# Optimization experiments

Hardware: AMD Instinct MI355X
Metric: run time of the kernel (lower is better)

Reference implementation:

```python
import jax, jax.numpy as jnp
import numpy as np

N = 100000       # num nodes
E = 1600000      # num edges (before self loops)
IN = 128         # in_channels
H = 4            # heads (layer 1)
C = 64           # hidden_channels
BN_EPS = 1e-5
NEG_SLOPE = 0.2  # PyG GATConv default


def setup_inputs() -> dict:
    key = jax.random.key(0)
    ks = jax.random.split(key, 12)
    s = lambda k, shape: jax.random.normal(k, shape, jnp.float32) * 0.05
    return {
        "x": jax.random.normal(ks[0], (N, IN), jnp.float32),
        "edge_index": jax.random.randint(ks[1], (2, E), 0, N),
        # GATConv layer 1: in=128 -> 64 per head, 4 heads, concat
        "W1": s(ks[2], (IN, H * C)),
        "a_src1": s(ks[3], (H, C)),
        "a_dst1": s(ks[4], (H, C)),
        "b1": jnp.zeros((H * C,), jnp.float32),
        # BatchNorm1d(256), eval mode with default running stats
        "bn_gamma": jnp.ones((H * C,), jnp.float32),
        "bn_beta": jnp.zeros((H * C,), jnp.float32),
        # GATConv layer 2: 256 -> 1, heads=1, concat=False
        "W2": s(ks[5], (H * C, 1)),
        "a_src2": s(ks[6], (1, 1)),
        "a_dst2": s(ks[7], (1, 1)),
        "b2": jnp.zeros((1,), jnp.float32),
        # risk predictor MLP: Linear(1,64) -> ReLU -> Linear(64,1) -> Sigmoid
        "mlp_w1": s(ks[8], (1, C)),
        "mlp_b1": jnp.zeros((C,), jnp.float32),
        "mlp_w2": s(ks[9], (C, 1)),
        "mlp_b2": jnp.zeros((1,), jnp.float32),
    }


def gat_conv(x, W, a_s, a_d, b, src, dst, n, concat):
    """PyG-style GATConv (self loops already appended to src/dst)."""
    h_, c_ = a_s.shape
    h = (x @ W).reshape(n, h_, c_)                       # [N,H,C]
    alpha_src = jnp.einsum('nhc,hc->nh', h, a_s)          # [N,H]
    alpha_dst = jnp.einsum('nhc,hc->nh', h, a_d)          # [N,H]
    alpha = jax.nn.leaky_relu(alpha_src[src] + alpha_dst[dst], NEG_SLOPE)  # [E,H]
    # segment softmax over destination nodes (self loops guarantee nonempty segments)
    amax = jax.ops.segment_max(alpha, dst, num_segments=n)
    ex = jnp.exp(alpha - amax[dst])
    den = jax.ops.segment_sum(ex, dst, num_segments=n)
    coef = ex / den[dst]                                  # [E,H]
    out = jax.ops.segment_sum(h[src] * coef[..., None], dst, num_segments=n)  # [N,H,C]
    out = out.reshape(n, h_ * c_) if concat else out.mean(axis=1)
    return out + b


def reference(x, edge_index, W1, a_src1, a_dst1, b1, bn_gamma, bn_beta,
              W2, a_src2, a_dst2, b2, mlp_w1, mlp_b1, mlp_w2, mlp_b2):
    n = x.shape[0]
    loops = jnp.arange(n)
    src = jnp.concatenate([edge_index[0], loops])
    dst = jnp.concatenate([edge_index[1], loops])

    h = gat_conv(x, W1, a_src1, a_dst1, b1, src, dst, n, concat=True)   # [N,256]
    # BatchNorm1d eval: running_mean=0, running_var=1
    h = h / jnp.sqrt(jnp.float32(1.0 + BN_EPS)) * bn_gamma + bn_beta
    h = jax.nn.elu(h)
    # dropout is identity in eval mode
    h = gat_conv(h, W2, a_src2, a_dst2, b2, src, dst, n, concat=False)  # [N,1]

    risk = jax.nn.relu(h @ mlp_w1 + mlp_b1)
    risk = jax.nn.sigmoid(risk @ mlp_w2 + mlp_b2)                        # [N,1]
    return risk
```

## Files before the change

### kernel.cpp

```cpp
#include <hip/hip_runtime.h>
#include <math.h>

#define NSL 0.2f
#define BSH 8
#define CAP 4608
#define ECHUNK 4096
#define MAXNB 512

typedef __attribute__((ext_vector_type(8))) short bf16x8;
typedef __attribute__((ext_vector_type(4))) float f32x4;
typedef __attribute__((ext_vector_type(2))) float floatx2;

__device__ __forceinline__ unsigned short f2b(float f){
  unsigned int u = __builtin_bit_cast(unsigned int, f);
  u = (u + 0x7FFFu + ((u >> 16) & 1u)) >> 16;
  return (unsigned short)u;
}
__device__ __forceinline__ unsigned cvtpk_bf16(float a, float b){
  unsigned r; asm("v_cvt_pk_bf16_f32 %0, %1, %2" : "=v"(r) : "v"(a), "v"(b)); return r;
}
__device__ __forceinline__ void pkfma(floatx2& a, floatx2 x, floatx2 w){
  asm("v_pk_fma_f32 %0, %1, %2, %0" : "+v"(a) : "v"(x), "v"(w));
}

__global__ void k_binit(int* gCur, int NB){
  int i = blockIdx.x*blockDim.x + threadIdx.x;
  if (i < NB) gCur[i] = i*CAP;
}

__global__ __launch_bounds__(256) void k_bucket(const int* __restrict__ esrc, const int* __restrict__ edst,
                                                int E, int NB, int* gCur, uint2* __restrict__ ebuf){
  __shared__ int hist[MAXNB];
  __shared__ int base[MAXNB];
  int t = threadIdx.x;
  for (int i=t;i<NB;i+=256) hist[i] = 0;
  __syncthreads();
  int e0 = blockIdx.x*ECHUNK;
  int srcv[16], dstv[16];
  #pragma unroll
  for (int j=0;j<16;j++){
    int e = e0 + t + j*256;
    if (e < E){ srcv[j] = esrc[e]; dstv[j] = edst[e]; atomicAdd(&hist[dstv[j]>>BSH], 1); }
    else dstv[j] = -1;
  }
  __syncthreads();
  for (int i=t;i<NB;i+=256){
    int h = hist[i];
    base[i] = h > 0 ? atomicAdd(&gCur[i], h) : 0;
    hist[i] = 0;
  }
  __syncthreads();
  #pragma unroll
  for (int j=0;j<16;j++){
    if (dstv[j] >= 0){
      int b = dstv[j]>>BSH;
      int pos = base[b] + atomicAdd(&hist[b], 1);
      if (pos < (b+1)*CAP)
        ebuf[pos] = (uint2){ (unsigned)srcv[j], (unsigned)dstv[j] };
    }
  }
}

__global__ __launch_bounds__(256) void k_csr(const int* __restrict__ gCur, const uint2* __restrict__ ebuf,
                                             int* __restrict__ rows, int* __restrict__ deg,
                                             int* __restrict__ csr, int N){
  __shared__ int lcnt[256];
  __shared__ int rofs[256];
  __shared__ int csr_l[CAP+256];
  int b = blockIdx.x, t = threadIdx.x;
  int node0 = b<<BSH;
  int nNodes = min(256, N - node0);
  int cnt_b = min(gCur[b] - b*CAP, CAP);
  lcnt[t] = 0;
  __syncthreads();
  const uint2* eb = ebuf + (size_t)b*CAP;
  for (int i=t;i<cnt_b;i+=256) atomicAdd(&lcnt[eb[i].y & 255], 1);
  __syncthreads();
  int v = (t < nNodes) ? (lcnt[t] + 1) : 0;
  rofs[t] = v; __syncthreads();
  #pragma unroll
  for (int o=1;o<256;o<<=1){
    int x = (t>=o) ? rofs[t-o] : 0; __syncthreads();
    rofs[t] += x; __syncthreads();
  }
  int excl = rofs[t] - v;
  if (t < nNodes) csr_l[excl] = node0 + t;
  lcnt[t] = excl + 1;
  __syncthreads();
  for (int i=t;i<cnt_b;i+=256){
    uint2 e = eb[i];
    int pos = atomicAdd(&lcnt[e.y & 255], 1);
    csr_l[pos] = (int)e.x;
  }
  __syncthreads();
  int total = rofs[255];
  int gbase = b*(CAP+256);
  for (int i=t;i<total;i+=256) csr[gbase+i] = csr_l[i];
  if (t < nNodes){ rows[node0+t] = gbase + excl; deg[node0+t] = v; }
}

__global__ __launch_bounds__(256) void k_prep_w(const float* __restrict__ W, unsigned short* __restrict__ wt){
  int idx = blockIdx.x*256 + threadIdx.x;
  int k = idx >> 8, ch = idx & 255;
  wt[ch*128 + k] = f2b(W[idx]);
}

__global__ __launch_bounds__(256) void k_gemm1(const unsigned short* __restrict__ w1t,
                                               const float* __restrict__ x,
                                               const float* __restrict__ a_s1,
                                               const float* __restrict__ a_d1,
                                               unsigned char* __restrict__ h1f8,
                                               float* __restrict__ asrc, float* __restrict__ adst,
                                               int N){
  __shared__ unsigned short xs[64][132];
  int tid = threadIdx.x;
  int lane = tid & 63, w = tid >> 6;
  int g = lane >> 4, nr = lane & 15;
  int n0 = blockIdx.x*64;

  #pragma unroll
  for (int i=0;i<8;i++){
    int idx = tid + i*256;
    int node = idx >> 5, c4 = idx & 31;
    int gn = n0 + node;
    float4 v = (gn < N) ? *(const float4*)&x[(size_t)gn*128 + c4*4] : make_float4(0,0,0,0);
    uint2 pk = { cvtpk_bf16(v.x, v.y), cvtpk_bf16(v.z, v.w) };
    *(uint2*)&xs[node][c4*4] = pk;
  }
  __syncthreads();

  int node_f[4]; bool val_f[4];
  #pragma unroll
  for (int fn=0;fn<4;fn++){ node_f[fn] = n0 + fn*16 + nr; val_f[fn] = node_f[fn] < N; }

  f32x4 acc[4][4] = {};
  #pragma unroll
  for (int s=0;s<4;s++){
    int ks = s*32;
    bf16x8 af[4], bf[4];
    #pragma unroll
    for (int fm=0;fm<4;fm++){
      int ch = w*64 + fm*16 + nr;
      const ushort4 lo = *(const ushort4*)(w1t + ch*128 + ks + 4*g);
      const ushort4 hi = *(const ushort4*)(w1t + ch*128 + ks + 16 + 4*g);
      af[fm] = (bf16x8){ (short)lo.x,(short)lo.y,(short)lo.z,(short)lo.w,
                         (short)hi.x,(short)hi.y,(short)hi.z,(short)hi.w };
    }
    #pragma unroll
    for (int fn=0;fn<4;fn++){
      union { uint2 u2[2]; bf16x8 v; } bb;
      bb.u2[0] = *(const uint2*)&xs[fn*16 + nr][ks + 4*g];
      bb.u2[1] = *(const uint2*)&xs[fn*16 + nr][ks + 16 + 4*g];
      bf[fn] = bb.v;
    }
    #pragma unroll
    for (int fm=0;fm<4;fm++)
      #pragma unroll
      for (int fn=0;fn<4;fn++)
        acc[fm][fn] = __builtin_amdgcn_mfma_f32_16x16x32_bf16(af[fm], bf[fn], acc[fm][fn], 0, 0, 0);
  }

  float ps[4] = {0.f,0.f,0.f,0.f}, pd[4] = {0.f,0.f,0.f,0.f};
  #pragma unroll
  for (int fm=0;fm<4;fm++){
    int cb = w*64 + fm*16 + g*4;
    float4 av = *(const float4*)&a_s1[cb];
    float4 dv = *(const float4*)&a_d1[cb];
    #pragma unroll
    for (int fn=0;fn<4;fn++){
      f32x4 c = acc[fm][fn];
      if (val_f[fn]){
        int u = __builtin_amdgcn_cvt_pk_fp8_f32(c[0], c[1], 0, false);
        u = __builtin_amdgcn_cvt_pk_fp8_f32(c[2], c[3], u, true);
        *(unsigned int*)(h1f8 + (size_t)node_f[fn]*256 + cb) = (unsigned int)u;
      }
      ps[fn] += c[0]*av.x + c[1]*av.y + c[2]*av.z + c[3]*av.w;
      pd[fn] += c[0]*dv.x + c[1]*dv.y + c[2]*dv.z + c[3]*dv.w;
    }
  }
  #pragma unroll
  for (int fn=0;fn<4;fn++){
    ps[fn] += __shfl_xor(ps[fn], 16); ps[fn] += __shfl_xor(ps[fn], 32);
    pd[fn] += __shfl_xor(pd[fn], 16); pd[fn] += __shfl_xor(pd[fn], 32);
    if (g == 0 && val_f[fn]){
      asrc[node_f[fn]*4 + w] = ps[fn];
      adst[node_f[fn]*4 + w] = pd[fn];
    }
  }
}

__global__ __launch_bounds__(256) void k_agg1(const int* __restrict__ rows, const int* __restrict__ deg,
                                              const int* __restrict__ csr,
                                              const unsigned char* __restrict__ h1f8,
                                              const float* __restrict__ asrc, const float* __restrict__ adst,
                                              const float* __restrict__ b1,
                                              const float* __restrict__ gamma, const float* __restrict__ beta,
                                              const float* __restrict__ W2,
                                              float* __restrict__ h2, int N){
  int lane = threadIdx.x & 63, wv = threadIdx.x >> 6;
  int node = blockIdx.x*4 + wv;
  if (node >= N) return;
  int slot = lane >> 4, l4 = lane & 15;
  int head = l4 >> 2;
  int rs = rows[node], d = deg[node];
  float adh = adst[node*4 + head];
  const uint4* h1u4 = (const uint4*)h1f8;
  floatx2 acc2[8];
  #pragma unroll
  for (int j=0;j<8;j++){ acc2[j][0] = 0.f; acc2[j][1] = 0.f; }
  float den = 0.f;
  int i = slot;
  if (i < d){
    int s = csr[rs+i];
    float aa = asrc[s*4 + head];
    uint4 v = h1u4[(size_t)s*16 + l4];
    while (true){
      int in = i + 4;
      bool hn = in < d;
      int sn = hn ? csr[rs+in] : 0;
      float al = aa + adh;
      al = fmaxf(al, NSL*al);
      float wgt = __expf(al);
      den += wgt;
      floatx2 ww; ww[0] = wgt; ww[1] = wgt;
      floatx2 f;
      f = __builtin_amdgcn_cvt_pk_f32_fp8(v.x, false); pkfma(acc2[0], f, ww);
      f = __builtin_amdgcn_cvt_pk_f32_fp8(v.x, true ); pkfma(acc2[1], f, ww);
      f = __builtin_amdgcn_cvt_pk_f32_fp8(v.y, false); pkfma(acc2[2], f, ww);
      f = __builtin_amdgcn_cvt_pk_f32_fp8(v.y, true ); pkfma(acc2[3], f, ww);
      f = __builtin_amdgcn_cvt_pk_f32_fp8(v.z, false); pkfma(acc2[4], f, ww);
      f = __builtin_amdgcn_cvt_pk_f32_fp8(v.z, true ); pkfma(acc2[5], f, ww);
      f = __builtin_amdgcn_cvt_pk_f32_fp8(v.w, false); pkfma(acc2[6], f, ww);
      f = __builtin_amdgcn_cvt_pk_f32_fp8(v.w, true ); pkfma(acc2[7], f, ww);
      if (!hn) break;
      i = in;
      aa = asrc[sn*4 + head];
      v = h1u4[(size_t)sn*16 + l4];
    }
  }
  #pragma unroll
  for (int j=0;j<8;j++){
    acc2[j][0] += __shfl_xor(acc2[j][0],16); acc2[j][1] += __shfl_xor(acc2[j][1],16);
    acc2[j][0] += __shfl_xor(acc2[j][0],32); acc2[j][1] += __shfl_xor(acc2[j][1],32);
  }
  den += __shfl_xor(den,16); den += __shfl_xor(den,32);
  float inv = 1.f/den;
  const float bsc = 0.99999500003749968f;
  int c = l4*16;
  float p = 0.f;
  #pragma unroll
  for (int q=0;q<4;q++){
    int cq = c + q*4;
    float4 bb = *(const float4*)&b1[cq];
    float4 gg = *(const float4*)&gamma[cq];
    float4 be = *(const float4*)&beta[cq];
    float4 w2 = *(const float4*)&W2[cq];
    float o0 = (acc2[q*2+0][0]*inv + bb.x)*bsc*gg.x + be.x;
    float o1 = (acc2[q*2+0][1]*inv + bb.y)*bsc*gg.y + be.y;
    float o2 = (acc2[q*2+1][0]*inv + bb.z)*bsc*gg.z + be.z;
    float o3 = (acc2[q*2+1][1]*inv + bb.w)*bsc*gg.w + be.w;
    o0 = (o0>0.f)?o0:(__expf(o0)-1.f); o1 = (o1>0.f)?o1:(__expf(o1)-1.f);
    o2 = (o2>0.f)?o2:(__expf(o2)-1.f); o3 = (o3>0.f)?o3:(__expf(o3)-1.f);
    p += o0*w2.x + o1*w2.y + o2*w2.z + o3*w2.w;
  }
  p += __shfl_xor(p,1); p += __shfl_xor(p,2); p += __shfl_xor(p,4); p += __shfl_xor(p,8);
  if (lane == 0) h2[node] = p;
}

__global__ __launch_bounds__(256) void k_agg2(const int* __restrict__ rows, const int* __restrict__ deg,
                       const int* __restrict__ csr, const float* __restrict__ h2,
                       const float* __restrict__ as2, const float* __restrict__ ad2,
                       const float* __restrict__ b2,
                       const float* __restrict__ mw1, const float* __restrict__ mb1,
                       const float* __restrict__ mw2, const float* __restrict__ mb2,
                       float* __restrict__ out, int N){
  int t = threadIdx.x;
  int g16 = t >> 4, l = t & 15;
  int n = blockIdx.x*16 + g16;
  if (n >= N) return;
  float a_s = as2[0], a_d = ad2[0];
  float hd = h2[n];
  float ad = hd * a_d;
  int rs = rows[n], d = deg[n];
  float den = 0.f, num = 0.f;
  for (int i=l;i<d;i+=16){
    int s = csr[rs+i];
    float hs = h2[s];
    float al = hs*a_s + ad;
    al = fmaxf(al, NSL*al);
    float w = __expf(al);
    den += w; num += w*hs;
  }
  #pragma unroll
  for (int o=1;o<16;o<<=1){ den += __shfl_xor(den,o); num += __shfl_xor(num,o); }
  float o2 = num/den + b2[0];
  float acc = 0.f;
  #pragma unroll
  for (int q=0;q<4;q++){
    int j = l + q*16;
    float r = fmaxf(o2*mw1[j] + mb1[j], 0.f);
    acc += r*mw2[j];
  }
  #pragma unroll
  for (int o=1;o<16;o<<=1) acc += __shfl_xor(acc,o);
  if (l == 0) out[n] = 1.f/(1.f + __expf(-(acc + mb2[0])));
}

extern "C" void kernel_launch(void* const* d_in, const int* in_sizes, int n_in,
                              void* d_out, int out_size, void* d_ws, size_t ws_size,
                              hipStream_t stream){
  const float* x   = (const float*)d_in[0];
  const int*   ei  = (const int*)  d_in[1];
  const float* W1  = (const float*)d_in[2];
  const float* as1 = (const float*)d_in[3];
  const float* ad1 = (const float*)d_in[4];
  const float* b1  = (const float*)d_in[5];
  const float* gam = (const float*)d_in[6];
  const float* bet = (const float*)d_in[7];
  const float* W2  = (const float*)d_in[8];
  const float* as2 = (const float*)d_in[9];
  const float* ad2 = (const float*)d_in[10];
  const float* b2  = (const float*)d_in[11];
  const float* mw1 = (const float*)d_in[12];
  const float* mb1 = (const float*)d_in[13];
  const float* mw2 = (const float*)d_in[14];
  const float* mb2 = (const float*)d_in[15];
  float* out = (float*)d_out;

  int N = in_sizes[0] / 128;
  int E = in_sizes[1] / 2;
  const int* esrc = ei;
  const int* edst = ei + E;
  int NB = (N + 255) >> 8;

  char* p = (char*)d_ws;
  auto alloc = [&](size_t bytes)->char*{ char* r = p; p += (bytes + 255) & ~(size_t)255; return r; };
  int*   deg   = (int*)  alloc((size_t)N*4);
  int*   rows  = (int*)  alloc((size_t)N*4);
  int*   gCur  = (int*)  alloc((size_t)NB*4);
  uint2* ebuf  = (uint2*)alloc((size_t)NB*CAP*8);
  int*   csr   = (int*)  alloc((size_t)NB*(CAP+256)*4);
  unsigned short* w1t  = (unsigned short*)alloc((size_t)256*128*2);
  unsigned char*  h1f8 = (unsigned char*) alloc((size_t)N*256);
  float* asrc  = (float*)alloc((size_t)N*4*4);
  float* adst  = (float*)alloc((size_t)N*4*4);
  float* h2    = (float*)alloc((size_t)N*4);

  k_binit<<<(NB+255)/256,256,0,stream>>>(gCur, NB);
  int nbA = (E + ECHUNK - 1)/ECHUNK;
  k_bucket<<<nbA,256,0,stream>>>(esrc, edst, E, NB, gCur, ebuf);
  k_csr   <<<NB,256,0,stream>>>(gCur, ebuf, rows, deg, csr, N);

  k_prep_w<<<128,256,0,stream>>>(W1, w1t);

  k_gemm1<<<(N+63)/64,256,0,stream>>>(w1t, x, as1, ad1, h1f8, asrc, adst, N);

  k_agg1 <<<(N+3)/4,256,0,stream>>>(rows, deg, csr, h1f8, asrc, adst, b1, gam, bet, W2, h2, N);

  k_agg2 <<<(N+15)/16,256,0,stream>>>(rows, deg, csr, h2, as2, ad2, b2, mw1, mb1, mw2, mb2, out, N);
}
```

Measured before the change: 225.4 us.

## Precompute per-edge attention weights in CSR build and deepen agg1 prefetch

Packs each bucketed edge into one 32-bit word (17-bit source plus 8-bit local destination), halving the edge buffer traffic. The CSR kernel now runs after the GEMM and computes the leaky-relu and exp attention weight for all four heads per edge, stored contiguously alongside the CSR. The first aggregation kernel reads these precomputed weights instead of gathering asrc per edge, and its loop becomes a two-deep software-pipelined prefetch. In exchange it adds a 16-byte-per-edge weight array write and read, and assumes node ids fit in 17 bits.

```diff
diff --git a/kernel.cpp b/kernel.cpp
--- a/kernel.cpp
+++ b/kernel.cpp
@@ -29,7 +29,7 @@
 }
 
 __global__ __launch_bounds__(256) void k_bucket(const int* __restrict__ esrc, const int* __restrict__ edst,
-                                                int E, int NB, int* gCur, uint2* __restrict__ ebuf){
+                                                int E, int NB, int* gCur, unsigned* __restrict__ ebuf){
   __shared__ int hist[MAXNB];
   __shared__ int base[MAXNB];
   int t = threadIdx.x;
@@ -56,25 +56,27 @@
       int b = dstv[j]>>BSH;
       int pos = base[b] + atomicAdd(&hist[b], 1);
       if (pos < (b+1)*CAP)
-        ebuf[pos] = (uint2){ (unsigned)srcv[j], (unsigned)dstv[j] };
-    }
-  }
-}
-
-__global__ __launch_bounds__(256) void k_csr(const int* __restrict__ gCur, const uint2* __restrict__ ebuf,
+        ebuf[pos] = (unsigned)srcv[j] | ((unsigned)(dstv[j] & 255) << 17);
+    }
+  }
+}
+
+__global__ __launch_bounds__(256) void k_csr(const int* __restrict__ gCur, const unsigned* __restrict__ ebuf,
+                                             const float* __restrict__ as4, const float* __restrict__ ad4,
                                              int* __restrict__ rows, int* __restrict__ deg,
-                                             int* __restrict__ csr, int N){
+                                             int* __restrict__ csr, float* __restrict__ wgt4, int N){
   __shared__ int lcnt[256];
   __shared__ int rofs[256];
   __shared__ int csr_l[CAP+256];
+  __shared__ unsigned char dl_l[CAP+256];
   int b = blockIdx.x, t = threadIdx.x;
   int node0 = b<<BSH;
   int nNodes = min(256, N - node0);
   int cnt_b = min(gCur[b] - b*CAP, CAP);
   lcnt[t] = 0;
   __syncthreads();
-  const uint2* eb = ebuf + (size_t)b*CAP;
-  for (int i=t;i<cnt_b;i+=256) atomicAdd(&lcnt[eb[i].y & 255], 1);
+  const unsigned* eb = ebuf + (size_t)b*CAP;
+  for (int i=t;i<cnt_b;i+=256) atomicAdd(&lcnt[eb[i]>>17], 1);
   __syncthreads();
   int v = (t < nNodes) ? (lcnt[t] + 1) : 0;
   rofs[t] = v; __syncthreads();
@@ -84,18 +86,31 @@
     rofs[t] += x; __syncthreads();
   }
   int excl = rofs[t] - v;
-  if (t < nNodes) csr_l[excl] = node0 + t;
+  if (t < nNodes){ csr_l[excl] = node0 + t; dl_l[excl] = (unsigned char)t; }
   lcnt[t] = excl + 1;
   __syncthreads();
   for (int i=t;i<cnt_b;i+=256){
-    uint2 e = eb[i];
-    int pos = atomicAdd(&lcnt[e.y & 255], 1);
-    csr_l[pos] = (int)e.x;
+    unsigned e = eb[i];
+    int dl = e >> 17;
+    int pos = atomicAdd(&lcnt[dl], 1);
+    csr_l[pos] = (int)(e & 0x1FFFFu);
+    dl_l[pos]  = (unsigned char)dl;
   }
   __syncthreads();
   int total = rofs[255];
   int gbase = b*(CAP+256);
-  for (int i=t;i<total;i+=256) csr[gbase+i] = csr_l[i];
+  for (int i=t;i<total;i+=256){
+    int src = csr_l[i];
+    int dl  = dl_l[i];
+    float4 av = *(const float4*)&as4[(size_t)src*4];
+    float4 dv = *(const float4*)&ad4[(size_t)(node0+dl)*4];
+    float ax = av.x+dv.x, ay = av.y+dv.y, az = av.z+dv.z, aw = av.w+dv.w;
+    ax = fmaxf(ax, NSL*ax); ay = fmaxf(ay, NSL*ay);
+    az = fmaxf(az, NSL*az); aw = fmaxf(aw, NSL*aw);
+    float4 w4 = { __expf(ax), __expf(ay), __expf(az), __expf(aw) };
+    *(float4*)&wgt4[(size_t)(gbase+i)*4] = w4;
+    csr[gbase+i] = src;
+  }
   if (t < nNodes){ rows[node0+t] = gbase + excl; deg[node0+t] = v; }
 }
 
@@ -191,8 +206,8 @@
 
 __global__ __launch_bounds__(256) void k_agg1(const int* __restrict__ rows, const int* __restrict__ deg,
                                               const int* __restrict__ csr,
+                                              const float* __restrict__ wgtf,
                                               const unsigned char* __restrict__ h1f8,
-                                              const float* __restrict__ asrc, const float* __restrict__ adst,
                                               const float* __restrict__ b1,
                                               const float* __restrict__ gamma, const float* __restrict__ beta,
                                               const float* __restrict__ W2,
@@ -203,41 +218,47 @@
   int slot = lane >> 4, l4 = lane & 15;
   int head = l4 >> 2;
   int rs = rows[node], d = deg[node];
-  float adh = adst[node*4 + head];
   const uint4* h1u4 = (const uint4*)h1f8;
   floatx2 acc2[8];
   #pragma unroll
   for (int j=0;j<8;j++){ acc2[j][0] = 0.f; acc2[j][1] = 0.f; }
   float den = 0.f;
-  int i = slot;
-  if (i < d){
-    int s = csr[rs+i];
-    float aa = asrc[s*4 + head];
-    uint4 v = h1u4[(size_t)s*16 + l4];
-    while (true){
-      int in = i + 4;
-      bool hn = in < d;
-      int sn = hn ? csr[rs+in] : 0;
-      float al = aa + adh;
-      al = fmaxf(al, NSL*al);
-      float wgt = __expf(al);
-      den += wgt;
-      floatx2 ww; ww[0] = wgt; ww[1] = wgt;
-      floatx2 f;
-      f = __builtin_amdgcn_cvt_pk_f32_fp8(v.x, false); pkfma(acc2[0], f, ww);
-      f = __builtin_amdgcn_cvt_pk_f32_fp8(v.x, true ); pkfma(acc2[1], f, ww);
-      f = __builtin_amdgcn_cvt_pk_f32_fp8(v.y, false); pkfma(acc2[2], f, ww);
-      f = __builtin_amdgcn_cvt_pk_f32_fp8(v.y, true ); pkfma(acc2[3], f, ww);
-      f = __builtin_amdgcn_cvt_pk_f32_fp8(v.z, false); pkfma(acc2[4], f, ww);
-      f = __builtin_amdgcn_cvt_pk_f32_fp8(v.z, true ); pkfma(acc2[5], f, ww);
-      f = __builtin_amdgcn_cvt_pk_f32_fp8(v.w, false); pkfma(acc2[6], f, ww);
-      f = __builtin_amdgcn_cvt_pk_f32_fp8(v.w, true ); pkfma(acc2[7], f, ww);
-      if (!hn) break;
-      i = in;
-      aa = asrc[sn*4 + head];
-      v = h1u4[(size_t)sn*16 + l4];
-    }
-  }
+  int nit = (d + 3) >> 2;
+
+  int i0 = slot;
+  bool ok0 = i0 < d;
+  int   s0 = ok0 ? csr[rs+i0] : 0;
+  float w0 = ok0 ? wgtf[(size_t)(rs+i0)*4 + head] : 0.f;
+  uint4 v0 = h1u4[(size_t)s0*16 + l4];
+  int i1 = i0 + 4;
+  bool ok1 = i1 < d;
+  int   s1 = ok1 ? csr[rs+i1] : 0;
+  float w1 = ok1 ? wgtf[(size_t)(rs+i1)*4 + head] : 0.f;
+  uint4 v1 = h1u4[(size_t)s1*16 + l4];
+
+  #pragma unroll 2
+  for (int it=0; it<nit; ++it){
+    int ip = i0 + 8;
+    bool okp = ip < d;
+    int   sp = okp ? csr[rs+ip] : 0;
+    float wp = okp ? wgtf[(size_t)(rs+ip)*4 + head] : 0.f;
+    uint4 vp = h1u4[(size_t)sp*16 + l4];
+    den += w0;
+    floatx2 ww; ww[0] = w0; ww[1] = w0;
+    floatx2 f;
+    f = __builtin_amdgcn_cvt_pk_f32_fp8(v0.x, false); pkfma(acc2[0], f, ww);
+    f = __builtin_amdgcn_cvt_pk_f32_fp8(v0.x, true ); pkfma(acc2[1], f, ww);
+    f = __builtin_amdgcn_cvt_pk_f32_fp8(v0.y, false); pkfma(acc2[2], f, ww);
+    f = __builtin_amdgcn_cvt_pk_f32_fp8(v0.y, true ); pkfma(acc2[3], f, ww);
+    f = __builtin_amdgcn_cvt_pk_f32_fp8(v0.z, false); pkfma(acc2[4], f, ww);
+    f = __builtin_amdgcn_cvt_pk_f32_fp8(v0.z, true ); pkfma(acc2[5], f, ww);
+    f = __builtin_amdgcn_cvt_pk_f32_fp8(v0.w, false); pkfma(acc2[6], f, ww);
+    f = __builtin_amdgcn_cvt_pk_f32_fp8(v0.w, true ); pkfma(acc2[7], f, ww);
+    s0 = s1; w0 = w1; v0 = v1;
+    s1 = sp; w1 = wp; v1 = vp;
+    i0 += 4;
+  }
+
   #pragma unroll
   for (int j=0;j<8;j++){
     acc2[j][0] += __shfl_xor(acc2[j][0],16); acc2[j][1] += __shfl_xor(acc2[j][1],16);
@@ -335,11 +356,12 @@
 
   char* p = (char*)d_ws;
   auto alloc = [&](size_t bytes)->char*{ char* r = p; p += (bytes + 255) & ~(size_t)255; return r; };
-  int*   deg   = (int*)  alloc((size_t)N*4);
-  int*   rows  = (int*)  alloc((size_t)N*4);
-  int*   gCur  = (int*)  alloc((size_t)NB*4);
-  uint2* ebuf  = (uint2*)alloc((size_t)NB*CAP*8);
-  int*   csr   = (int*)  alloc((size_t)NB*(CAP+256)*4);
+  int*      deg   = (int*)     alloc((size_t)N*4);
+  int*      rows  = (int*)     alloc((size_t)N*4);
+  int*      gCur  = (int*)     alloc((size_t)NB*4);
+  unsigned* ebuf  = (unsigned*)alloc((size_t)NB*CAP*4);
+  int*      csr   = (int*)     alloc((size_t)NB*(CAP+256)*4);
+  float*    wgt4  = (float*)   alloc((size_t)NB*(CAP+256)*16);
   unsigned short* w1t  = (unsigned short*)alloc((size_t)256*128*2);
   unsigned char*  h1f8 = (unsigned char*) alloc((size_t)N*256);
   float* asrc  = (float*)alloc((size_t)N*4*4);
@@ -349,13 +371,13 @@
   k_binit<<<(NB+255)/256,256,0,stream>>>(gCur, NB);
   int nbA = (E + ECHUNK - 1)/ECHUNK;
   k_bucket<<<nbA,256,0,stream>>>(esrc, edst, E, NB, gCur, ebuf);
-  k_csr   <<<NB,256,0,stream>>>(gCur, ebuf, rows, deg, csr, N);
 
   k_prep_w<<<128,256,0,stream>>>(W1, w1t);
-
   k_gemm1<<<(N+63)/64,256,0,stream>>>(w1t, x, as1, ad1, h1f8, asrc, adst, N);
 
-  k_agg1 <<<(N+3)/4,256,0,stream>>>(rows, deg, csr, h1f8, asrc, adst, b1, gam, bet, W2, h2, N);
-
-  k_agg2 <<<(N+15)/16,256,0,stream>>>(rows, deg, csr, h2, as2, ad2, b2, mw1, mb1, mw2, mb2, out, N);
-}
+  k_csr<<<NB,256,0,stream>>>(gCur, ebuf, asrc, adst, rows, deg, csr, wgt4, N);
+
+  k_agg1<<<(N+3)/4,256,0,stream>>>(rows, deg, csr, wgt4, h1f8, b1, gam, bet, W2, h2, N);
+
+  k_agg2<<<(N+15)/16,256,0,stream>>>(rows, deg, csr, h2, as2, ad2, b2, mw1, mb1, mw2, mb2, out, N);
+}
```

New measurement: 237.9 us. +5.6%, slower.

## Fuse independent prep kernels into horizontally combined launches and pack bucketed edges

Applied to the files above, without the earlier changes.

Merges the weight transpose with edge bucketing, and the GEMM with CSR construction, into two launches that split work by block index. The init kernel becomes a memset with per-bucket relative offsets. Bucketed edges are packed into 32 bits (source plus local destination), which halves the staging buffer traffic. This removes launch gaps and lets independent work overlap. The cost is a union shared-memory footprint sized for the larger CSR branch, which may reduce GEMM occupancy, and a packing that assumes node ids fit in 17 bits.

```diff
diff --git a/kernel.cpp b/kernel.cpp
--- a/kernel.cpp
+++ b/kernel.cpp
@@ -23,19 +23,23 @@
   asm("v_pk_fma_f32 %0, %1, %2, %0" : "+v"(a) : "v"(x), "v"(w));
 }
 
-__global__ void k_binit(int* gCur, int NB){
-  int i = blockIdx.x*blockDim.x + threadIdx.x;
-  if (i < NB) gCur[i] = i*CAP;
-}
-
-__global__ __launch_bounds__(256) void k_bucket(const int* __restrict__ esrc, const int* __restrict__ edst,
-                                                int E, int NB, int* gCur, uint2* __restrict__ ebuf){
+__global__ __launch_bounds__(256) void k_fused1(const float* __restrict__ W, unsigned short* __restrict__ wt,
+                                                const int* __restrict__ esrc, const int* __restrict__ edst,
+                                                int E, int NB, int* gCur, unsigned* __restrict__ ebuf,
+                                                int prepBlocks){
   __shared__ int hist[MAXNB];
   __shared__ int base[MAXNB];
-  int t = threadIdx.x;
+  int bid = blockIdx.x, t = threadIdx.x;
+  if (bid < prepBlocks){
+    int idx = bid*256 + t;
+    int k = idx >> 8, ch = idx & 255;
+    wt[ch*128 + k] = f2b(W[idx]);
+    return;
+  }
+  int b0 = bid - prepBlocks;
   for (int i=t;i<NB;i+=256) hist[i] = 0;
   __syncthreads();
-  int e0 = blockIdx.x*ECHUNK;
+  int e0 = b0*ECHUNK;
   int srcv[16], dstv[16];
   #pragma unroll
   for (int j=0;j<16;j++){
@@ -55,137 +59,133 @@
     if (dstv[j] >= 0){
       int b = dstv[j]>>BSH;
       int pos = base[b] + atomicAdd(&hist[b], 1);
-      if (pos < (b+1)*CAP)
-        ebuf[pos] = (uint2){ (unsigned)srcv[j], (unsigned)dstv[j] };
-    }
-  }
-}
-
-__global__ __launch_bounds__(256) void k_csr(const int* __restrict__ gCur, const uint2* __restrict__ ebuf,
-                                             int* __restrict__ rows, int* __restrict__ deg,
-                                             int* __restrict__ csr, int N){
-  __shared__ int lcnt[256];
-  __shared__ int rofs[256];
-  __shared__ int csr_l[CAP+256];
-  int b = blockIdx.x, t = threadIdx.x;
-  int node0 = b<<BSH;
-  int nNodes = min(256, N - node0);
-  int cnt_b = min(gCur[b] - b*CAP, CAP);
-  lcnt[t] = 0;
-  __syncthreads();
-  const uint2* eb = ebuf + (size_t)b*CAP;
-  for (int i=t;i<cnt_b;i+=256) atomicAdd(&lcnt[eb[i].y & 255], 1);
-  __syncthreads();
-  int v = (t < nNodes) ? (lcnt[t] + 1) : 0;
-  rofs[t] = v; __syncthreads();
-  #pragma unroll
-  for (int o=1;o<256;o<<=1){
-    int x = (t>=o) ? rofs[t-o] : 0; __syncthreads();
-    rofs[t] += x; __syncthreads();
-  }
-  int excl = rofs[t] - v;
-  if (t < nNodes) csr_l[excl] = node0 + t;
-  lcnt[t] = excl + 1;
-  __syncthreads();
-  for (int i=t;i<cnt_b;i+=256){
-    uint2 e = eb[i];
-    int pos = atomicAdd(&lcnt[e.y & 255], 1);
-    csr_l[pos] = (int)e.x;
-  }
-  __syncthreads();
-  int total = rofs[255];
-  int gbase = b*(CAP+256);
-  for (int i=t;i<total;i+=256) csr[gbase+i] = csr_l[i];
-  if (t < nNodes){ rows[node0+t] = gbase + excl; deg[node0+t] = v; }
-}
-
-__global__ __launch_bounds__(256) void k_prep_w(const float* __restrict__ W, unsigned short* __restrict__ wt){
-  int idx = blockIdx.x*256 + threadIdx.x;
-  int k = idx >> 8, ch = idx & 255;
-  wt[ch*128 + k] = f2b(W[idx]);
-}
-
-__global__ __launch_bounds__(256) void k_gemm1(const unsigned short* __restrict__ w1t,
-                                               const float* __restrict__ x,
-                                               const float* __restrict__ a_s1,
-                                               const float* __restrict__ a_d1,
-                                               unsigned char* __restrict__ h1f8,
-                                               float* __restrict__ asrc, float* __restrict__ adst,
-                                               int N){
-  __shared__ unsigned short xs[64][132];
+      if (pos < CAP)
+        ebuf[(size_t)b*CAP + pos] = (unsigned)srcv[j] | ((unsigned)(dstv[j] & 255) << 17);
+    }
+  }
+}
+
+__global__ __launch_bounds__(256) void k_fused2(const unsigned short* __restrict__ w1t,
+                                                const float* __restrict__ x,
+                                                const float* __restrict__ a_s1,
+                                                const float* __restrict__ a_d1,
+                                                unsigned char* __restrict__ h1f8,
+                                                float* __restrict__ asrc, float* __restrict__ adst,
+                                                int N, int gemmBlocks,
+                                                const int* __restrict__ gCur, const unsigned* __restrict__ ebuf,
+                                                int* __restrict__ rows, int* __restrict__ deg,
+                                                int* __restrict__ csr){
+  __shared__ union SM {
+    unsigned short xs[64][132];
+    struct { int lcnt[256]; int rofs[256]; int csr_l[CAP+256]; } c;
+  } sm;
   int tid = threadIdx.x;
-  int lane = tid & 63, w = tid >> 6;
-  int g = lane >> 4, nr = lane & 15;
-  int n0 = blockIdx.x*64;
-
-  #pragma unroll
-  for (int i=0;i<8;i++){
-    int idx = tid + i*256;
-    int node = idx >> 5, c4 = idx & 31;
-    int gn = n0 + node;
-    float4 v = (gn < N) ? *(const float4*)&x[(size_t)gn*128 + c4*4] : make_float4(0,0,0,0);
-    uint2 pk = { cvtpk_bf16(v.x, v.y), cvtpk_bf16(v.z, v.w) };
-    *(uint2*)&xs[node][c4*4] = pk;
-  }
-  __syncthreads();
-
-  int node_f[4]; bool val_f[4];
-  #pragma unroll
-  for (int fn=0;fn<4;fn++){ node_f[fn] = n0 + fn*16 + nr; val_f[fn] = node_f[fn] < N; }
-
-  f32x4 acc[4][4] = {};
-  #pragma unroll
-  for (int s=0;s<4;s++){
-    int ks = s*32;
-    bf16x8 af[4], bf[4];
+  int bid = blockIdx.x;
+
+  if (bid < gemmBlocks){
+    int lane = tid & 63, w = tid >> 6;
+    int g = lane >> 4, nr = lane & 15;
+    int n0 = bid*64;
+    #pragma unroll
+    for (int i=0;i<8;i++){
+      int idx = tid + i*256;
+      int node = idx >> 5, c4 = idx & 31;
+      int gn = n0 + node;
+      float4 v = (gn < N) ? *(const float4*)&x[(size_t)gn*128 + c4*4] : make_float4(0,0,0,0);
+      uint2 pk = { cvtpk_bf16(v.x, v.y), cvtpk_bf16(v.z, v.w) };
+      *(uint2*)&sm.xs[node][c4*4] = pk;
+    }
+    __syncthreads();
+
+    int node_f[4]; bool val_f[4];
+    #pragma unroll
+    for (int fn=0;fn<4;fn++){ node_f[fn] = n0 + fn*16 + nr; val_f[fn] = node_f[fn] < N; }
+
+    f32x4 acc[4][4] = {};
+    #pragma unroll
+    for (int s=0;s<4;s++){
+      int ks = s*32;
+      bf16x8 af[4], bf[4];
+      #pragma unroll
+      for (int fm=0;fm<4;fm++){
+        int ch = w*64 + fm*16 + nr;
+        const ushort4 lo = *(const ushort4*)(w1t + ch*128 + ks + 4*g);
+        const ushort4 hi = *(const ushort4*)(w1t + ch*128 + ks + 16 + 4*g);
+        af[fm] = (bf16x8){ (short)lo.x,(short)lo.y,(short)lo.z,(short)lo.w,
+                           (short)hi.x,(short)hi.y,(short)hi.z,(short)hi.w };
+      }
+      #pragma unroll
+      for (int fn=0;fn<4;fn++){
+        union { uint2 u2[2]; bf16x8 v; } bb;
+        bb.u2[0] = *(const uint2*)&sm.xs[fn*16 + nr][ks + 4*g];
+        bb.u2[1] = *(const uint2*)&sm.xs[fn*16 + nr][ks + 16 + 4*g];
+        bf[fn] = bb.v;
+      }
+      #pragma unroll
+      for (int fm=0;fm<4;fm++)
+        #pragma unroll
+        for (int fn=0;fn<4;fn++)
+          acc[fm][fn] = __builtin_amdgcn_mfma_f32_16x16x32_bf16(af[fm], bf[fn], acc[fm][fn], 0, 0, 0);
+    }
+
+    float ps[4] = {0.f,0.f,0.f,0.f}, pd[4] = {0.f,0.f,0.f,0.f};
     #pragma unroll
     for (int fm=0;fm<4;fm++){
-      int ch = w*64 + fm*16 + nr;
-      const ushort4 lo = *(const ushort4*)(w1t + ch*128 + ks + 4*g);
-      const ushort4 hi = *(const ushort4*)(w1t + ch*128 + ks + 16 + 4*g);
-      af[fm] = (bf16x8){ (short)lo.x,(short)lo.y,(short)lo.z,(short)lo.w,
-                         (short)hi.x,(short)hi.y,(short)hi.z,(short)hi.w };
+      int cb = w*64 + fm*16 + g*4;
+      float4 av = *(const float4*)&a_s1[cb];
+      float4 dv = *(const float4*)&a_d1[cb];
+      #pragma unroll
+      for (int fn=0;fn<4;fn++){
+        f32x4 c = acc[fm][fn];
+        if (val_f[fn]){
+          int u = __builtin_amdgcn_cvt_pk_fp8_f32(c[0], c[1], 0, false);
+          u = __builtin_amdgcn_cvt_pk_fp8_f32(c[2], c[3], u, true);
+          *(unsigned int*)(h1f8 + (size_t)node_f[fn]*256 + cb) = (unsigned int)u;
+        }
+        ps[fn] += c[0]*av.x + c[1]*av.y + c[2]*av.z + c[3]*av.w;
+        pd[fn] += c[0]*dv.x + c[1]*dv.y + c[2]*dv.z + c[3]*dv.w;
+      }
     }
     #pragma unroll
     for (int fn=0;fn<4;fn++){
-      union { uint2 u2[2]; bf16x8 v; } bb;
-      bb.u2[0] = *(const uint2*)&xs[fn*16 + nr][ks + 4*g];
-      bb.u2[1] = *(const uint2*)&xs[fn*16 + nr][ks + 16 + 4*g];
-      bf[fn] = bb.v;
-    }
-    #pragma unroll
-    for (int fm=0;fm<4;fm++)
-      #pragma unroll
-      for (int fn=0;fn<4;fn++)
-        acc[fm][fn] = __builtin_amdgcn_mfma_f32_16x16x32_bf16(af[fm], bf[fn], acc[fm][fn], 0, 0, 0);
-  }
-
-  float ps[4] = {0.f,0.f,0.f,0.f}, pd[4] = {0.f,0.f,0.f,0.f};
-  #pragma unroll
-  for (int fm=0;fm<4;fm++){
-    int cb = w*64 + fm*16 + g*4;
-    float4 av = *(const float4*)&a_s1[cb];
-    float4 dv = *(const float4*)&a_d1[cb];
-    #pragma unroll
-    for (int fn=0;fn<4;fn++){
-      f32x4 c = acc[fm][fn];
-      if (val_f[fn]){
-        int u = __builtin_amdgcn_cvt_pk_fp8_f32(c[0], c[1], 0, false);
-        u = __builtin_amdgcn_cvt_pk_fp8_f32(c[2], c[3], u, true);
-        *(unsigned int*)(h1f8 + (size_t)node_f[fn]*256 + cb) = (unsigned int)u;
+      ps[fn] += __shfl_xor(ps[fn], 16); ps[fn] += __shfl_xor(ps[fn], 32);
+      pd[fn] += __shfl_xor(pd[fn], 16); pd[fn] += __shfl_xor(pd[fn], 32);
+      if (g == 0 && val_f[fn]){
+        asrc[node_f[fn]*4 + w] = ps[fn];
+        adst[node_f[fn]*4 + w] = pd[fn];
       }
-      ps[fn] += c[0]*av.x + c[1]*av.y + c[2]*av.z + c[3]*av.w;
-      pd[fn] += c[0]*dv.x + c[1]*dv.y + c[2]*dv.z + c[3]*dv.w;
-    }
-  }
-  #pragma unroll
-  for (int fn=0;fn<4;fn++){
-    ps[fn] += __shfl_xor(ps[fn], 16); ps[fn] += __shfl_xor(ps[fn], 32);
-    pd[fn] += __shfl_xor(pd[fn], 16); pd[fn] += __shfl_xor(pd[fn], 32);
-    if (g == 0 && val_f[fn]){
-      asrc[node_f[fn]*4 + w] = ps[fn];
-      adst[node_f[fn]*4 + w] = pd[fn];
-    }
+    }
+  } else {
+    int b = bid - gemmBlocks;
+    int node0 = b<<BSH;
+    int nNodes = min(256, N - node0);
+    int cnt_b = min(gCur[b], CAP);
+    sm.c.lcnt[tid] = 0;
+    __syncthreads();
+    const unsigned* eb = ebuf + (size_t)b*CAP;
+    for (int i=tid;i<cnt_b;i+=256) atomicAdd(&sm.c.lcnt[eb[i]>>17], 1);
+    __syncthreads();
+    int v = (tid < nNodes) ? (sm.c.lcnt[tid] + 1) : 0;
+    sm.c.rofs[tid] = v; __syncthreads();
+    #pragma unroll
+    for (int o=1;o<256;o<<=1){
+      int xv = (tid>=o) ? sm.c.rofs[tid-o] : 0; __syncthreads();
+      sm.c.rofs[tid] += xv; __syncthreads();
+    }
+    int excl = sm.c.rofs[tid] - v;
+    if (tid < nNodes) sm.c.csr_l[excl] = node0 + tid;
+    sm.c.lcnt[tid] = excl + 1;
+    __syncthreads();
+    for (int i=tid;i<cnt_b;i+=256){
+      unsigned e = eb[i];
+      int pos = atomicAdd(&sm.c.lcnt[e>>17], 1);
+      sm.c.csr_l[pos] = (int)(e & 0x1FFFFu);
+    }
+    __syncthreads();
+    int total = sm.c.rofs[255];
+    int gbase = b*(CAP+256);
+    for (int i=tid;i<total;i+=256) csr[gbase+i] = sm.c.csr_l[i];
+    if (tid < nNodes){ rows[node0+tid] = gbase + excl; deg[node0+tid] = v; }
   }
 }
 
@@ -254,14 +254,14 @@
     float4 bb = *(const float4*)&b1[cq];
     float4 gg = *(const float4*)&gamma[cq];
     float4 be = *(const float4*)&beta[cq];
-    float4 w2 = *(const float4*)&W2[cq];
+    float4 w2_ = *(const float4*)&W2[cq];
     float o0 = (acc2[q*2+0][0]*inv + bb.x)*bsc*gg.x + be.x;
     float o1 = (acc2[q*2+0][1]*inv + bb.y)*bsc*gg.y + be.y;
     float o2 = (acc2[q*2+1][0]*inv + bb.z)*bsc*gg.z + be.z;
     float o3 = (acc2[q*2+1][1]*inv + bb.w)*bsc*gg.w + be.w;
     o0 = (o0>0.f)?o0:(__expf(o0)-1.f); o1 = (o1>0.f)?o1:(__expf(o1)-1.f);
     o2 = (o2>0.f)?o2:(__expf(o2)-1.f); o3 = (o3>0.f)?o3:(__expf(o3)-1.f);
-    p += o0*w2.x + o1*w2.y + o2*w2.z + o3*w2.w;
+    p += o0*w2_.x + o1*w2_.y + o2*w2_.z + o3*w2_.w;
   }
   p += __shfl_xor(p,1); p += __shfl_xor(p,2); p += __shfl_xor(p,4); p += __shfl_xor(p,8);
   if (lane == 0) h2[node] = p;
@@ -335,27 +335,28 @@
 
   char* p = (char*)d_ws;
   auto alloc = [&](size_t bytes)->char*{ char* r = p; p += (bytes + 255) & ~(size_t)255; return r; };
-  int*   deg   = (int*)  alloc((size_t)N*4);
-  int*   rows  = (int*)  alloc((size_t)N*4);
-  int*   gCur  = (int*)  alloc((size_t)NB*4);
-  uint2* ebuf  = (uint2*)alloc((size_t)NB*CAP*8);
-  int*   csr   = (int*)  alloc((size_t)NB*(CAP+256)*4);
+  int*      deg   = (int*)     alloc((size_t)N*4);
+  int*      rows  = (int*)     alloc((size_t)N*4);
+  int*      gCur  = (int*)     alloc((size_t)NB*4);
+  unsigned* ebuf  = (unsigned*)alloc((size_t)NB*CAP*4);
+  int*      csr   = (int*)     alloc((size_t)NB*(CAP+256)*4);
   unsigned short* w1t  = (unsigned short*)alloc((size_t)256*128*2);
   unsigned char*  h1f8 = (unsigned char*) alloc((size_t)N*256);
   float* asrc  = (float*)alloc((size_t)N*4*4);
   float* adst  = (float*)alloc((size_t)N*4*4);
   float* h2    = (float*)alloc((size_t)N*4);
 
-  k_binit<<<(NB+255)/256,256,0,stream>>>(gCur, NB);
+  hipMemsetAsync(gCur, 0, (size_t)NB*4, stream);
+
+  int prepBlocks = 128;
   int nbA = (E + ECHUNK - 1)/ECHUNK;
-  k_bucket<<<nbA,256,0,stream>>>(esrc, edst, E, NB, gCur, ebuf);
-  k_csr   <<<NB,256,0,stream>>>(gCur, ebuf, rows, deg, csr, N);
-
-  k_prep_w<<<128,256,0,stream>>>(W1, w1t);
-
-  k_gemm1<<<(N+63)/64,256,0,stream>>>(w1t, x, as1, ad1, h1f8, asrc, adst, N);
-
-  k_agg1 <<<(N+3)/4,256,0,stream>>>(rows, deg, csr, h1f8, asrc, adst, b1, gam, bet, W2, h2, N);
-
-  k_agg2 <<<(N+15)/16,256,0,stream>>>(rows, deg, csr, h2, as2, ad2, b2, mw1, mb1, mw2, mb2, out, N);
-}
+  k_fused1<<<prepBlocks + nbA, 256, 0, stream>>>(W1, w1t, esrc, edst, E, NB, gCur, ebuf, prepBlocks);
+
+  int gemmBlocks = (N + 63)/64;
+  k_fused2<<<gemmBlocks + NB, 256, 0, stream>>>(w1t, x, as1, ad1, h1f8, asrc, adst,
+                                                N, gemmBlocks, gCur, ebuf, rows, deg, csr);
+
+  k_agg1<<<(N+3)/4,256,0,stream>>>(rows, deg, csr, h1f8, asrc, adst, b1, gam, bet, W2, h2, N);
+
+  k_agg2<<<(N+15)/16,256,0,stream>>>(rows, deg, csr, h2, as2, ad2, b2, mw1, mb1, mw2, mb2, out, N);
+}
```

Measured after the change: 217.3 us, median of 2. 3.6% less time.
